# Kernel tuning notes

Measured on AMD Instinct MI355X. Metric: run time of the kernel, lower is better.

Reference implementation:

```python
import jax, jax.numpy as jnp
import numpy as np

NEG_SLOPE = 0.2
EPS_SOFTMAX = 1e-16
EPS_NORM = 1e-12
H = 4


def gat_conv(x, src, dst, edge_attr, W, att_src, att_dst, W_edge, att_edge, bias, concat):
    """PyG GATConv with edge_dim, add_self_loops=False.
    x: [N, F_in]; src,dst: [E]; edge_attr: [E, edge_dim]
    W: [F_in, H*C]; att_src/att_dst/att_edge: [H, C]; W_edge: [edge_dim, H*C]
    """
    N = x.shape[0]
    C = att_src.shape[1]
    xs = (x @ W).reshape(N, H, C)                      # [N,H,C]
    a_s = jnp.einsum('nhc,hc->nh', xs, att_src)        # [N,H]
    a_d = jnp.einsum('nhc,hc->nh', xs, att_dst)        # [N,H]
    e = (edge_attr @ W_edge).reshape(-1, H, C)         # [E,H,C]
    a_e = jnp.einsum('ehc,hc->eh', e, att_edge)        # [E,H]
    alpha = a_s[src] + a_d[dst] + a_e                  # [E,H]
    alpha = jax.nn.leaky_relu(alpha, NEG_SLOPE)
    # segment softmax over edges grouped by destination node
    m = jax.ops.segment_max(alpha, dst, num_segments=N)        # [N,H]
    ex = jnp.exp(alpha - m[dst])
    denom = jax.ops.segment_sum(ex, dst, num_segments=N)       # [N,H]
    alpha = ex / (denom[dst] + EPS_SOFTMAX)
    # message = attention-weighted source features, scatter-add to dst
    out = jax.ops.segment_sum(xs[src] * alpha[..., None], dst, num_segments=N)  # [N,H,C]
    out = out.reshape(N, H * C) if concat else out.mean(axis=1)
    return out + bias


def l2_normalize(x):
    n = jnp.linalg.norm(x, axis=-1, keepdims=True)
    return x / jnp.maximum(n, EPS_NORM)


def setup_inputs() -> dict:
    key = jax.random.key(0)
    ks = jax.random.split(key, 16)
    N, E, F_in, C1, C2 = 50000, 800000, 128, 64, 64
    glorot = lambda k, shape: jax.random.uniform(
        k, shape, jnp.float32, -1.0, 1.0) * np.sqrt(6.0 / (shape[0] + shape[-1]))
    return {
        'x': jax.random.normal(ks[0], (N, F_in), jnp.float32),
        'edge_index': jax.random.randint(ks[1], (2, E), 0, N, jnp.int32),
        'edge_weight': jax.random.uniform(ks[2], (E, 1), jnp.float32),
        # layer 1: in=128 -> H*C1=256, concat=True
        'W1': glorot(ks[3], (F_in, H * C1)),
        'att_src1': glorot(ks[4], (H, C1)),
        'att_dst1': glorot(ks[5], (H, C1)),
        'We1': glorot(ks[6], (1, H * C1)),
        'att_e1': glorot(ks[7], (H, C1)),
        'b1': jnp.zeros((H * C1,), jnp.float32),
        # layer 2: in=256 -> H*C2, concat=False (mean over heads)
        'W2': glorot(ks[8], (H * C1, H * C2)),
        'att_src2': glorot(ks[9], (H, C2)),
        'att_dst2': glorot(ks[10], (H, C2)),
        'We2': glorot(ks[11], (1, H * C2)),
        'att_e2': glorot(ks[12], (H, C2)),
        'b2': jnp.zeros((C2,), jnp.float32),
    }


def reference(x, edge_index, edge_weight, W1, att_src1, att_dst1, We1, att_e1, b1,
              W2, att_src2, att_dst2, We2, att_e2, b2):
    src, dst = edge_index[0], edge_index[1]
    h = gat_conv(x, src, dst, edge_weight, W1, att_src1, att_dst1, We1, att_e1, b1, concat=True)
    h = jax.nn.relu(l2_normalize(h))
    out = gat_conv(h, src, dst, edge_weight, W2, att_src2, att_dst2, We2, att_e2, b2, concat=False)
    return out
```

## Files before the change

kernel.cpp:

```cpp
#include <hip/hip_runtime.h>
#include <hip/hip_bf16.h>

typedef unsigned short u16;
typedef unsigned long long u64;
using bf16x8 = __attribute__((ext_vector_type(8))) short;
using f32x4v = __attribute__((ext_vector_type(4))) float;
typedef float v2f __attribute__((ext_vector_type(2)));

#define HC 256
#define CDIM 64

__device__ __forceinline__ float b2f(u16 u){
  union { unsigned int i; float f; } c; c.i = ((unsigned)u) << 16; return c.f;
}
__device__ __forceinline__ u16 f2b(float f){
  union { float f; unsigned int i; } c; c.f = f;
  unsigned int x = c.i;
  return (u16)((x + 0x7FFFu + ((x >> 16) & 1u)) >> 16);
}
__device__ __forceinline__ float ldf(const void* p, size_t i, int isbf){
  return isbf ? b2f(((const u16*)p)[i]) : ((const float*)p)[i];
}
__device__ __forceinline__ float sel4(float4 v, int h){ return h==0?v.x:(h==1?v.y:(h==2?v.z:v.w)); }
__device__ __forceinline__ float lrelu(float v){ return v>0.f ? v : 0.2f*v; }

__device__ __forceinline__ void glds16(const void* g, void* l){
  __builtin_amdgcn_global_load_lds(
      (const __attribute__((address_space(1))) unsigned int*)g,
      (__attribute__((address_space(3))) unsigned int*)l, 16, 0, 0);
}

__device__ __forceinline__ float4 wave_max4(float4 m){
  #pragma unroll
  for(int o=32;o>0;o>>=1){
    m.x=fmaxf(m.x,__shfl_xor(m.x,o));
    m.y=fmaxf(m.y,__shfl_xor(m.y,o));
    m.z=fmaxf(m.z,__shfl_xor(m.z,o));
    m.w=fmaxf(m.w,__shfl_xor(m.w,o));
  }
  return m;
}
__device__ __forceinline__ float4 wave_sum4(float4 m){
  #pragma unroll
  for(int o=32;o>0;o>>=1){
    m.x+=__shfl_xor(m.x,o);
    m.y+=__shfl_xor(m.y,o);
    m.z+=__shfl_xor(m.z,o);
    m.w+=__shfl_xor(m.w,o);
  }
  return m;
}

__global__ void k_hist(const int* __restrict__ dst, int E, int N, int* __restrict__ deg,
                       int* __restrict__ rank,
                       const u16* __restrict__ x, int nelem, int* __restrict__ flag){
  int e = blockIdx.x*256 + threadIdx.x;
  if (e < E){
    int d = dst[e];
    if ((unsigned)d < (unsigned)N) rank[e] = atomicAdd(&deg[d], 1);
  }
  if (blockIdx.x == 0){
    __shared__ int bad;
    if (threadIdx.x==0) bad = 0;
    __syncthreads();
    int n = nelem < 8192 ? nelem : 8192;
    int localbad = 0;
    for (int i=threadIdx.x; i<n; i+=256){
      int ex = (x[i] >> 7) & 0xFF;
      if (ex >= 140) localbad++;
    }
    if (localbad) atomicAdd(&bad, 1);
    __syncthreads();
    if (threadIdx.x==0) *flag = (bad==0) ? 1 : 0;
  }
}

__global__ void k_scan1(const int* __restrict__ in, int* __restrict__ out, int* __restrict__ bsums, int n){
  __shared__ int s[256];
  int t = threadIdx.x;
  int i = blockIdx.x*256 + t;
  int v = (i<n)? in[i] : 0;
  s[t]=v; __syncthreads();
  for(int off=1; off<256; off<<=1){
    int tv = (t>=off)? s[t-off] : 0;
    __syncthreads();
    s[t]+=tv; __syncthreads();
  }
  if (i<n) out[i] = s[t]-v;
  if (t==255) bsums[blockIdx.x] = s[255];
}

__global__ void k_scan2(int* __restrict__ bsums, int nb){
  __shared__ int s[256];
  int t=threadIdx.x;
  int v=(t<nb)? bsums[t]:0;
  s[t]=v; __syncthreads();
  for(int off=1; off<256; off<<=1){
    int tv=(t>=off)? s[t-off]:0;
    __syncthreads();
    s[t]+=tv; __syncthreads();
  }
  if (t<nb) bsums[t]=s[t]-v;
}

__global__ void k_scatter(const int* __restrict__ src, const int* __restrict__ dst,
                          const void* __restrict__ ew, int E, int N,
                          const int* __restrict__ rowptr, const int* __restrict__ bsums,
                          const int* __restrict__ rank, u64* __restrict__ epk,
                          const int* __restrict__ flagp){
  int e = blockIdx.x*256+threadIdx.x;
  if (e>=E) return;
  int bf = *flagp;
  int d = dst[e];
  if ((unsigned)d >= (unsigned)N) return;
  int p = rowptr[d] + bsums[d>>8] + rank[e];
  int s = src[e];
  if ((unsigned)s >= (unsigned)N) s = 0;
  u64 v = ((u64)__float_as_uint(ldf(ew, e, bf)) << 32) | (unsigned)s;
  __builtin_nontemporal_store(v, &epk[p]);
}

__global__ void k_prep(const void* __restrict__ W1, const void* __restrict__ W2,
                       const void* __restrict__ We1, const void* __restrict__ ae1,
                       const void* __restrict__ We2, const void* __restrict__ ae2,
                       u16* __restrict__ Bt1, u16* __restrict__ Bt2, float* __restrict__ ce,
                       const int* __restrict__ flagp){
  int bf = *flagp;
  int b = blockIdx.x, t = threadIdx.x;
  if (b < 128){
    Bt1[(size_t)t*128 + b] = f2b(ldf(W1, (size_t)b*HC + t, bf));
  } else if (b < 384){
    int k = b - 128;
    Bt2[(size_t)t*256 + k] = f2b(ldf(W2, (size_t)k*HC + t, bf));
  } else {
    float p1 = ldf(We1, t, bf)*ldf(ae1, t, bf);
    float p2 = ldf(We2, t, bf)*ldf(ae2, t, bf);
    #pragma unroll
    for(int o=32;o>0;o>>=1){ p1+=__shfl_xor(p1,o); p2+=__shfl_xor(p2,o); }
    if((t&63)==0){ ce[t>>6]=p1; ce[4+(t>>6)]=p2; }
  }
}

__global__ __launch_bounds__(256) void k_gemm_mfma(
    const void* __restrict__ A, int a_ext, const u16* __restrict__ Bt,
    u16* __restrict__ C, const void* __restrict__ att_s, const void* __restrict__ att_d,
    float* __restrict__ a_s, float* __restrict__ a_d,
    int M, int K, const int* __restrict__ flagp)
{
  __shared__ u16 sh[64*264];
  __shared__ float att_sh[512];
  u16* As = sh;
  u16* Bs = sh + 2048;
  int bf = *flagp;
  int a_bf = a_ext ? bf : 1;
  int tid = threadIdx.x;
  int lane = tid & 63, w = tid >> 6;
  int quad = lane >> 4, ln = lane & 15;
  int m0 = blockIdx.x * 64;

  att_sh[tid]       = ldf(att_s, tid, bf);
  att_sh[256 + tid] = ldf(att_d, tid, bf);

  f32x4v acc[4][4] = {};
  for (int k0 = 0; k0 < K; k0 += 32){
    if (!a_ext){
      const u16* gA = (const u16*)A + (size_t)(m0 + (tid>>2))*K + k0 + (size_t)(tid&3)*8;
      glds16(gA, (char*)As + (size_t)w*1024);
    } else {
      int m = tid >> 2, g = tid & 3;
      int r = m0 + m;
      uint4 pack;
      if (r < M){
        size_t base = (size_t)r*K + k0 + g*8;
        if (a_bf){
          pack = *(const uint4*)((const u16*)A + base);
        } else {
          const float* Af = (const float*)A + base;
          float4 f0 = *(const float4*)Af;
          float4 f1 = *(const float4*)(Af+4);
          unsigned a0 = (unsigned)f2b(f0.x) | ((unsigned)f2b(f0.y)<<16);
          unsigned a1 = (unsigned)f2b(f0.z) | ((unsigned)f2b(f0.w)<<16);
          unsigned a2 = (unsigned)f2b(f1.x) | ((unsigned)f2b(f1.y)<<16);
          unsigned a3 = (unsigned)f2b(f1.z) | ((unsigned)f2b(f1.w)<<16);
          pack = make_uint4(a0,a1,a2,a3);
        }
      } else pack = make_uint4(0,0,0,0);
      ((uint4*)As)[tid] = pack;
    }
    #pragma unroll
    for (int i=0;i<4;i++){
      const u16* gB = Bt + (size_t)(i*64 + (tid>>2))*K + k0 + (size_t)(tid&3)*8;
      glds16(gB, (char*)Bs + (size_t)i*4096 + (size_t)w*1024);
    }
    __syncthreads();
    bf16x8 af[4], bfr[4];
    #pragma unroll
    for (int mi=0;mi<4;mi++) af[mi] = *(const bf16x8*)&As[(mi*16+ln)*32 + quad*8];
    #pragma unroll
    for (int nj=0;nj<4;nj++) bfr[nj] = *(const bf16x8*)&Bs[((size_t)w*64+nj*16+ln)*32 + quad*8];
    #pragma unroll
    for (int mi=0;mi<4;mi++)
      #pragma unroll
      for (int nj=0;nj<4;nj++)
        acc[mi][nj] = __builtin_amdgcn_mfma_f32_16x16x32_bf16(af[mi], bfr[nj], acc[mi][nj], 0,0,0);
    __syncthreads();
  }
  #pragma unroll
  for (int mi=0;mi<4;mi++)
    #pragma unroll
    for (int nj=0;nj<4;nj++){
      union { __hip_bfloat162 h2; u16 u[2]; } cv0, cv1;
      cv0.h2 = __float22bfloat162_rn(make_float2(acc[mi][nj][0], acc[mi][nj][1]));
      cv1.h2 = __float22bfloat162_rn(make_float2(acc[mi][nj][2], acc[mi][nj][3]));
      int col = w*64 + nj*16 + ln;
      int rbase = mi*16 + quad*4;
      sh[(rbase+0)*264 + col] = cv0.u[0];
      sh[(rbase+1)*264 + col] = cv0.u[1];
      sh[(rbase+2)*264 + col] = cv1.u[0];
      sh[(rbase+3)*264 + col] = cv1.u[1];
    }
  __syncthreads();
  #pragma unroll
  for (int j=0;j<8;j++){
    int idx = j*256 + tid;
    int r = idx >> 5, gq = idx & 31;
    if (m0 + r < M)
      *(uint4*)(C + (size_t)(m0+r)*HC + gq*8) = *(const uint4*)&sh[r*264 + gq*8];
  }
  {
    int r  = w*16 + ln;
    int hh = quad;
    const u16* crow = &sh[r*264 + hh*64];
    const float* asv = &att_sh[hh*64];
    const float* adv = &att_sh[256 + hh*64];
    float ps = 0.f, pd = 0.f;
    #pragma unroll
    for (int cb=0; cb<64; cb+=8){
      ushort4 ua = *(const ushort4*)&crow[cb];
      ushort4 ub = *(const ushort4*)&crow[cb+4];
      float4 sa = *(const float4*)&asv[cb];
      float4 sb = *(const float4*)&asv[cb+4];
      float4 da = *(const float4*)&adv[cb];
      float4 db = *(const float4*)&adv[cb+4];
      float c0=b2f(ua.x), c1=b2f(ua.y), c2=b2f(ua.z), c3=b2f(ua.w);
      float c4=b2f(ub.x), c5=b2f(ub.y), c6=b2f(ub.z), c7=b2f(ub.w);
      ps += c0*sa.x + c1*sa.y + c2*sa.z + c3*sa.w + c4*sb.x + c5*sb.y + c6*sb.z + c7*sb.w;
      pd += c0*da.x + c1*da.y + c2*da.z + c3*da.w + c4*db.x + c5*db.y + c6*db.z + c7*db.w;
    }
    if (m0 + r < M){
      a_s[(size_t)(m0+r)*4 + hh] = ps;
      a_d[(size_t)(m0+r)*4 + hh] = pd;
    }
  }
}

#define GRP4(E0, TWJ) { \
  int s0_=__builtin_amdgcn_readlane(s_reg,(E0)+0); \
  int s1_=__builtin_amdgcn_readlane(s_reg,(E0)+1); \
  int s2_=__builtin_amdgcn_readlane(s_reg,(E0)+2); \
  int s3_=__builtin_amdgcn_readlane(s_reg,(E0)+3); \
  uint2 x0_=*(const uint2*)&xs[(size_t)s0_*HC + (lane<<2)]; \
  uint2 x1_=*(const uint2*)&xs[(size_t)s1_*HC + (lane<<2)]; \
  uint2 x2_=*(const uint2*)&xs[(size_t)s2_*HC + (lane<<2)]; \
  uint2 x3_=*(const uint2*)&xs[(size_t)s3_*HC + (lane<<2)]; \
  float w0_=__shfl((TWJ), ibase+(((E0)+0)&15)); \
  float w1_=__shfl((TWJ), ibase+(((E0)+1)&15)); \
  float w2_=__shfl((TWJ), ibase+(((E0)+2)&15)); \
  float w3_=__shfl((TWJ), ibase+(((E0)+3)&15)); \
  v2f f_; \
  f_=(v2f){__uint_as_float(x0_.x<<16),__uint_as_float(x0_.x&0xFFFF0000u)}; a01+=f_*w0_; \
  f_=(v2f){__uint_as_float(x0_.y<<16),__uint_as_float(x0_.y&0xFFFF0000u)}; a23+=f_*w0_; \
  f_=(v2f){__uint_as_float(x1_.x<<16),__uint_as_float(x1_.x&0xFFFF0000u)}; a01+=f_*w1_; \
  f_=(v2f){__uint_as_float(x1_.y<<16),__uint_as_float(x1_.y&0xFFFF0000u)}; a23+=f_*w1_; \
  f_=(v2f){__uint_as_float(x2_.x<<16),__uint_as_float(x2_.x&0xFFFF0000u)}; a01+=f_*w2_; \
  f_=(v2f){__uint_as_float(x2_.y<<16),__uint_as_float(x2_.y&0xFFFF0000u)}; a23+=f_*w2_; \
  f_=(v2f){__uint_as_float(x3_.x<<16),__uint_as_float(x3_.x&0xFFFF0000u)}; a01+=f_*w3_; \
  f_=(v2f){__uint_as_float(x3_.y<<16),__uint_as_float(x3_.y&0xFFFF0000u)}; a23+=f_*w3_; \
}

__global__ __launch_bounds__(256) void k_soft_agg(
    const u16* __restrict__ xs, const int* __restrict__ rowptr, const int* __restrict__ bsums,
    const int* __restrict__ deg, const u64* __restrict__ epk,
    const float* __restrict__ a_s, const float* __restrict__ a_d, const float* __restrict__ ce4,
    const void* __restrict__ bias, void* __restrict__ outp, int N, int layer,
    const int* __restrict__ flagp){
  int bf = *flagp;
  int lane = threadIdx.x & 63;
  int w = threadIdx.x >> 6;
  int n = (blockIdx.x<<2) + w;
  if (n >= N) return;
  int row = rowptr[n] + bsums[n>>8];
  int dg = deg[n];
  float4 ad = *(const float4*)&a_d[(size_t)n*4];
  float4 ce = *(const float4*)ce4;
  int h = lane >> 4;
  float4 acc = make_float4(0.f,0.f,0.f,0.f);
  if (dg > 0){
    if (dg <= 64){
      u64 pk = 0;
      if (lane < dg) pk = epk[row + lane];
      int s = (int)(unsigned)(pk & 0xFFFFFFFFull);
      if ((unsigned)s >= (unsigned)N) s = 0;
      int s_reg = s;
      float wv = __uint_as_float((unsigned)(pk >> 32));
      float4 as4 = *(const float4*)&a_s[(size_t)s*4];
      uint2 xpf[8];
      #pragma unroll
      for (int k=0;k<8;k++){
        int sk = __builtin_amdgcn_readlane(s_reg, k);
        xpf[k] = *(const uint2*)&xs[(size_t)sk*HC + (lane<<2)];
      }
      bool vlane = lane < dg;
      float4 ex;
      ex.x = vlane ? __expf(lrelu(as4.x+ad.x+wv*ce.x)) : 0.f;
      ex.y = vlane ? __expf(lrelu(as4.y+ad.y+wv*ce.y)) : 0.f;
      ex.z = vlane ? __expf(lrelu(as4.z+ad.z+wv*ce.z)) : 0.f;
      ex.w = vlane ? __expf(lrelu(as4.w+ad.w+wv*ce.w)) : 0.f;
      float4 ss = ex;
      if (dg > 32){
        ss.x+=__shfl_xor(ss.x,32); ss.y+=__shfl_xor(ss.y,32);
        ss.z+=__shfl_xor(ss.z,32); ss.w+=__shfl_xor(ss.w,32);
      }
      if (dg > 16){
        ss.x+=__shfl_xor(ss.x,16); ss.y+=__shfl_xor(ss.y,16);
        ss.z+=__shfl_xor(ss.z,16); ss.w+=__shfl_xor(ss.w,16);
      }
      #pragma unroll
      for(int o=8;o>0;o>>=1){
        ss.x+=__shfl_xor(ss.x,o); ss.y+=__shfl_xor(ss.y,o);
        ss.z+=__shfl_xor(ss.z,o); ss.w+=__shfl_xor(ss.w,o);
      }
      float4 wgt;
      wgt.x = ex.x/(ss.x+1e-16f); wgt.y = ex.y/(ss.y+1e-16f);
      wgt.z = ex.z/(ss.z+1e-16f); wgt.w = ex.w/(ss.w+1e-16f);
      int ibase = lane & 48;
      float tw0, tw1, tw2, tw3;
      {
        int srcl = lane & 15;
        float c0=__shfl(wgt.x,srcl), c1=__shfl(wgt.y,srcl);
        float c2=__shfl(wgt.z,srcl), c3=__shfl(wgt.w,srcl);
        tw0 = (h==0)?c0:((h==1)?c1:((h==2)?c2:c3));
      }
      if (dg > 16){
        int srcl = 16 + (lane & 15);
        float c0=__shfl(wgt.x,srcl), c1=__shfl(wgt.y,srcl);
        float c2=__shfl(wgt.z,srcl), c3=__shfl(wgt.w,srcl);
        tw1 = (h==0)?c0:((h==1)?c1:((h==2)?c2:c3));
      } else tw1 = 0.f;
      if (dg > 32){
        int srcl = 32 + (lane & 15);
        float c0=__shfl(wgt.x,srcl), c1=__shfl(wgt.y,srcl);
        float c2=__shfl(wgt.z,srcl), c3=__shfl(wgt.w,srcl);
        tw2 = (h==0)?c0:((h==1)?c1:((h==2)?c2:c3));
      } else tw2 = 0.f;
      if (dg > 48){
        int srcl = 48 + (lane & 15);
        float c0=__shfl(wgt.x,srcl), c1=__shfl(wgt.y,srcl);
        float c2=__shfl(wgt.z,srcl), c3=__shfl(wgt.w,srcl);
        tw3 = (h==0)?c0:((h==1)?c1:((h==2)?c2:c3));
      } else tw3 = 0.f;
      v2f a01 = {0.f,0.f}, a23 = {0.f,0.f};
      #pragma unroll
      for (int k=0;k<8;k++){
        float wk = __shfl(tw0, ibase+k);
        uint2 xv = xpf[k];
        v2f f;
        f = (v2f){__uint_as_float(xv.x<<16), __uint_as_float(xv.x&0xFFFF0000u)}; a01 += f*wk;
        f = (v2f){__uint_as_float(xv.y<<16), __uint_as_float(xv.y&0xFFFF0000u)}; a23 += f*wk;
      }
      if (dg >  8) GRP4( 8, tw0);
      if (dg > 12) GRP4(12, tw0);
      if (dg > 16){
        GRP4(16, tw1);
        if (dg > 20) GRP4(20, tw1);
        if (dg > 24) GRP4(24, tw1);
        if (dg > 28) GRP4(28, tw1);
        if (dg > 32){
          GRP4(32, tw2);
          if (dg > 36) GRP4(36, tw2);
          if (dg > 40) GRP4(40, tw2);
          if (dg > 44) GRP4(44, tw2);
          if (dg > 48){
            GRP4(48, tw3);
            if (dg > 52) GRP4(52, tw3);
            if (dg > 56) GRP4(56, tw3);
            if (dg > 60) GRP4(60, tw3);
          }
        }
      }
      acc.x = a01.x; acc.y = a01.y; acc.z = a23.x; acc.w = a23.y;
    } else {
      float4 m = make_float4(-1e30f,-1e30f,-1e30f,-1e30f);
      for (int p=lane;p<dg;p+=64){
        u64 pk = epk[row+p];
        int s = (int)(unsigned)(pk & 0xFFFFFFFFull);
        if ((unsigned)s >= (unsigned)N) s = 0;
        float wv = __uint_as_float((unsigned)(pk >> 32));
        float4 as = *(const float4*)&a_s[(size_t)s*4];
        m.x=fmaxf(m.x, lrelu(as.x+ad.x+wv*ce.x));
        m.y=fmaxf(m.y, lrelu(as.y+ad.y+wv*ce.y));
        m.z=fmaxf(m.z, lrelu(as.z+ad.z+wv*ce.z));
        m.w=fmaxf(m.w, lrelu(as.w+ad.w+wv*ce.w));
      }
      m = wave_max4(m);
      float4 ss = make_float4(0.f,0.f,0.f,0.f);
      for (int p=lane;p<dg;p+=64){
        u64 pk = epk[row+p];
        int s = (int)(unsigned)(pk & 0xFFFFFFFFull);
        if ((unsigned)s >= (unsigned)N) s = 0;
        float wv = __uint_as_float((unsigned)(pk >> 32));
        float4 as = *(const float4*)&a_s[(size_t)s*4];
        ss.x+=__expf(lrelu(as.x+ad.x+wv*ce.x)-m.x);
        ss.y+=__expf(lrelu(as.y+ad.y+wv*ce.y)-m.y);
        ss.z+=__expf(lrelu(as.z+ad.z+wv*ce.z)-m.z);
        ss.w+=__expf(lrelu(as.w+ad.w+wv*ce.w)-m.w);
      }
      ss = wave_sum4(ss);
      float rsel=1.f/(sel4(ss,h)+1e-16f), mh=sel4(m,h), adh=sel4(ad,h), ceh=sel4(ce,h);
      for (int e=0;e<dg;e++){
        u64 pk = epk[row+e];
        int s = (int)(unsigned)(pk & 0xFFFFFFFFull);
        if ((unsigned)s >= (unsigned)N) s = 0;
        float wv = __uint_as_float((unsigned)(pk >> 32));
        float arv = lrelu(a_s[(size_t)s*4+h]+adh+wv*ceh);
        float wgt = __expf(arv-mh)*rsel;
        ushort4 xv4 = *(const ushort4*)&xs[(size_t)s*HC + lane*4];
        acc.x+=wgt*b2f(xv4.x); acc.y+=wgt*b2f(xv4.y);
        acc.z+=wgt*b2f(xv4.z); acc.w+=wgt*b2f(xv4.w);
      }
    }
  }
  if (layer==1){
    float4 v;
    v.x = acc.x + ldf(bias, lane*4+0, bf);
    v.y = acc.y + ldf(bias, lane*4+1, bf);
    v.z = acc.z + ldf(bias, lane*4+2, bf);
    v.w = acc.w + ldf(bias, lane*4+3, bf);
    float ss = v.x*v.x+v.y*v.y+v.z*v.z+v.w*v.w;
    #pragma unroll
    for(int o=32;o>0;o>>=1) ss += __shfl_xor(ss,o);
    float inv = 1.f/fmaxf(sqrtf(ss), 1e-12f);
    ushort4 o4;
    o4.x = f2b(fmaxf(v.x*inv,0.f)); o4.y = f2b(fmaxf(v.y*inv,0.f));
    o4.z = f2b(fmaxf(v.z*inv,0.f)); o4.w = f2b(fmaxf(v.w*inv,0.f));
    *(ushort4*)((u16*)outp + (size_t)n*HC + lane*4) = o4;
  } else {
    float4 s = acc;
    #pragma unroll
    for (int o=16;o<=32;o<<=1){
      s.x+=__shfl_xor(s.x,o); s.y+=__shfl_xor(s.y,o);
      s.z+=__shfl_xor(s.z,o); s.w+=__shfl_xor(s.w,o);
    }
    if (lane < 16){
      float4 v;
      v.x = 0.25f*s.x + ldf(bias, lane*4+0, bf);
      v.y = 0.25f*s.y + ldf(bias, lane*4+1, bf);
      v.z = 0.25f*s.z + ldf(bias, lane*4+2, bf);
      v.w = 0.25f*s.w + ldf(bias, lane*4+3, bf);
      if (bf){
        ushort4 o4; o4.x=f2b(v.x); o4.y=f2b(v.y); o4.z=f2b(v.z); o4.w=f2b(v.w);
        *(ushort4*)((u16*)outp + (size_t)n*CDIM + lane*4) = o4;
      } else {
        *(float4*)((float*)outp + (size_t)n*CDIM + lane*4) = v;
      }
    }
  }
}

extern "C" void kernel_launch(void* const* d_in, const int* in_sizes, int n_in,
                              void* d_out, int out_size, void* d_ws, size_t ws_size,
                              hipStream_t stream){
  const void* x_in = d_in[0];
  const int* eidx  = (const int*)d_in[1];
  const void* ew   = d_in[2];
  const void* W1   = d_in[3];
  const void* as1  = d_in[4];
  const void* ad1  = d_in[5];
  const void* We1  = d_in[6];
  const void* ae1  = d_in[7];
  const void* b1   = d_in[8];
  const void* W2   = d_in[9];
  const void* as2  = d_in[10];
  const void* ad2  = d_in[11];
  const void* We2  = d_in[12];
  const void* ae2  = d_in[13];
  const void* b2   = d_in[14];

  int N = in_sizes[0]/128;
  int E = in_sizes[2];
  const int* src = eidx;
  const int* dst = eidx + E;

  char* w = (char*)d_ws;
  auto alloc = [&](size_t bytes)->char*{ char* p=w; w += (bytes+255)/256*256; return p; };
  int*   flag  = (int*)alloc(256);
  u16*   xs    = (u16*)alloc((size_t)N*HC*2);
  u16*   agg   = (u16*)alloc((size_t)N*HC*2);
  float* a_s   = (float*)alloc((size_t)N*4*4);
  float* a_d   = (float*)alloc((size_t)N*4*4);
  int*   deg   = (int*)alloc((size_t)N*4);
  int*   rowptr= (int*)alloc((size_t)N*4);
  int*   bsums = (int*)alloc(256*4);
  int*   rank  = (int*)alloc((size_t)E*4);
  u64*   epk   = (u64*)alloc((size_t)E*8);
  float* ce    = (float*)alloc(256);
  u16*   Bt1   = (u16*)alloc((size_t)HC*128*2);
  u16*   Bt2   = (u16*)alloc((size_t)HC*HC*2);

  (void)hipMemsetAsync(deg, 0, (size_t)N*4, stream);

  int eb = (E+255)/256;
  int nb = (N+255)/256;
  k_hist<<<eb,256,0,stream>>>(dst, E, N, deg, rank, (const u16*)x_in, in_sizes[0], flag);
  k_scan1<<<nb,256,0,stream>>>(deg, rowptr, bsums, N);
  k_scan2<<<1,256,0,stream>>>(bsums, nb);
  k_scatter<<<eb,256,0,stream>>>(src, dst, ew, E, N, rowptr, bsums, rank, epk, flag);
  k_prep<<<385,256,0,stream>>>(W1, W2, We1, ae1, We2, ae2, Bt1, Bt2, ce, flag);

  int gemmBlocks = (N+63)/64;
  int nwb = (N+3)/4;

  k_gemm_mfma<<<gemmBlocks,256,0,stream>>>(x_in, 1, Bt1, xs, as1, ad1, a_s, a_d, N, 128, flag);
  k_soft_agg<<<nwb,256,0,stream>>>(xs, rowptr, bsums, deg, epk, a_s, a_d, ce, b1, agg, N, 1, flag);

  k_gemm_mfma<<<gemmBlocks,256,0,stream>>>(agg, 0, Bt2, xs, as2, ad2, a_s, a_d, N, 256, flag);
  k_soft_agg<<<nwb,256,0,stream>>>(xs, rowptr, bsums, deg, epk, a_s, a_d, ce+4, b2, d_out, N, 2, flag);
}
```

Measured before the change: 328.5 us.

## Split waves into half-wave edge pairs with 16-byte gathers; fuse prep into hist

The soft-aggregation kernel now has each half-wave handle alternate edges, with every lane gathering 8 bf16 features (16 bytes) instead of 4. The two halves are combined with a cross-half shuffle at the end, and the block size drops to 128 threads (2 nodes per block). The aim is fewer, wider gather instructions and more edges in flight per wave, at the cost of extra reduction shuffles and ds_bpermute weight broadcasts. Separately, the weight-prep kernel is merged into the histogram kernel to save a launch, and the GEMM uses the direct global-to-LDS load path for bf16 inputs on full tiles.

Result: slower. 343.5 us (+4.6%).

```diff
diff --git a/kernel.cpp b/kernel.cpp
--- a/kernel.cpp
+++ b/kernel.cpp
@@ -23,6 +23,9 @@
 }
 __device__ __forceinline__ float sel4(float4 v, int h){ return h==0?v.x:(h==1?v.y:(h==2?v.z:v.w)); }
 __device__ __forceinline__ float lrelu(float v){ return v>0.f ? v : 0.2f*v; }
+__device__ __forceinline__ float wshf(float v, int addr4){
+  return __int_as_float(__builtin_amdgcn_ds_bpermute(addr4, __float_as_int(v)));
+}
 
 __device__ __forceinline__ void glds16(const void* g, void* l){
   __builtin_amdgcn_global_load_lds(
@@ -51,27 +54,63 @@
   return m;
 }
 
-__global__ void k_hist(const int* __restrict__ dst, int E, int N, int* __restrict__ deg,
-                       int* __restrict__ rank,
-                       const u16* __restrict__ x, int nelem, int* __restrict__ flag){
-  int e = blockIdx.x*256 + threadIdx.x;
-  if (e < E){
-    int d = dst[e];
-    if ((unsigned)d < (unsigned)N) rank[e] = atomicAdd(&deg[d], 1);
-  }
-  if (blockIdx.x == 0){
-    __shared__ int bad;
-    if (threadIdx.x==0) bad = 0;
-    __syncthreads();
+__global__ void k_hist_prep(const int* __restrict__ dst, int E, int N, int* __restrict__ deg,
+                            int* __restrict__ rank,
+                            const u16* __restrict__ x, int nelem, int* __restrict__ flag,
+                            const void* __restrict__ W1, const void* __restrict__ W2,
+                            const void* __restrict__ We1, const void* __restrict__ ae1,
+                            const void* __restrict__ We2, const void* __restrict__ ae2,
+                            u16* __restrict__ Bt1, u16* __restrict__ Bt2, float* __restrict__ ce){
+  int eb = (E + 255) >> 8;
+  int t = threadIdx.x;
+  if ((int)blockIdx.x < eb){
+    int e = blockIdx.x*256 + t;
+    if (e < E){
+      int d = dst[e];
+      if ((unsigned)d < (unsigned)N) rank[e] = atomicAdd(&deg[d], 1);
+    }
+    if (blockIdx.x == 0){
+      __shared__ int bad0;
+      if (t==0) bad0 = 0;
+      __syncthreads();
+      int n = nelem < 8192 ? nelem : 8192;
+      int localbad = 0;
+      for (int i=t; i<n; i+=256){
+        int ex = (x[i] >> 7) & 0xFF;
+        if (ex >= 140) localbad++;
+      }
+      if (localbad) atomicAdd(&bad0, 1);
+      __syncthreads();
+      if (t==0) *flag = (bad0==0) ? 1 : 0;
+    }
+    return;
+  }
+  __shared__ int bad;
+  if (t==0) bad = 0;
+  __syncthreads();
+  {
     int n = nelem < 8192 ? nelem : 8192;
     int localbad = 0;
-    for (int i=threadIdx.x; i<n; i+=256){
+    for (int i=t; i<n; i+=256){
       int ex = (x[i] >> 7) & 0xFF;
       if (ex >= 140) localbad++;
     }
     if (localbad) atomicAdd(&bad, 1);
-    __syncthreads();
-    if (threadIdx.x==0) *flag = (bad==0) ? 1 : 0;
+  }
+  __syncthreads();
+  int bf = (bad==0) ? 1 : 0;
+  int b = blockIdx.x - eb;
+  if (b < 128){
+    Bt1[(size_t)t*128 + b] = f2b(ldf(W1, (size_t)b*HC + t, bf));
+  } else if (b < 384){
+    int k = b - 128;
+    Bt2[(size_t)t*256 + k] = f2b(ldf(W2, (size_t)k*HC + t, bf));
+  } else {
+    float p1 = ldf(We1, t, bf)*ldf(ae1, t, bf);
+    float p2 = ldf(We2, t, bf)*ldf(ae2, t, bf);
+    #pragma unroll
+    for(int o=32;o>0;o>>=1){ p1+=__shfl_xor(p1,o); p2+=__shfl_xor(p2,o); }
+    if((t&63)==0){ ce[t>>6]=p1; ce[4+(t>>6)]=p2; }
   }
 }
 
@@ -118,27 +157,6 @@
   if ((unsigned)s >= (unsigned)N) s = 0;
   u64 v = ((u64)__float_as_uint(ldf(ew, e, bf)) << 32) | (unsigned)s;
   __builtin_nontemporal_store(v, &epk[p]);
-}
-
-__global__ void k_prep(const void* __restrict__ W1, const void* __restrict__ W2,
-                       const void* __restrict__ We1, const void* __restrict__ ae1,
-                       const void* __restrict__ We2, const void* __restrict__ ae2,
-                       u16* __restrict__ Bt1, u16* __restrict__ Bt2, float* __restrict__ ce,
-                       const int* __restrict__ flagp){
-  int bf = *flagp;
-  int b = blockIdx.x, t = threadIdx.x;
-  if (b < 128){
-    Bt1[(size_t)t*128 + b] = f2b(ldf(W1, (size_t)b*HC + t, bf));
-  } else if (b < 384){
-    int k = b - 128;
-    Bt2[(size_t)t*256 + k] = f2b(ldf(W2, (size_t)k*HC + t, bf));
-  } else {
-    float p1 = ldf(We1, t, bf)*ldf(ae1, t, bf);
-    float p2 = ldf(We2, t, bf)*ldf(ae2, t, bf);
-    #pragma unroll
-    for(int o=32;o>0;o>>=1){ p1+=__shfl_xor(p1,o); p2+=__shfl_xor(p2,o); }
-    if((t&63)==0){ ce[t>>6]=p1; ce[4+(t>>6)]=p2; }
-  }
 }
 
 __global__ __launch_bounds__(256) void k_gemm_mfma(
@@ -157,13 +175,14 @@
   int lane = tid & 63, w = tid >> 6;
   int quad = lane >> 4, ln = lane & 15;
   int m0 = blockIdx.x * 64;
+  bool adma = (!a_ext) || (a_bf && (m0 + 64 <= M));
 
   att_sh[tid]       = ldf(att_s, tid, bf);
   att_sh[256 + tid] = ldf(att_d, tid, bf);
 
   f32x4v acc[4][4] = {};
   for (int k0 = 0; k0 < K; k0 += 32){
-    if (!a_ext){
+    if (adma){
       const u16* gA = (const u16*)A + (size_t)(m0 + (tid>>2))*K + k0 + (size_t)(tid&3)*8;
       glds16(gA, (char*)As + (size_t)w*1024);
     } else {
@@ -254,31 +273,23 @@
   }
 }
 
-#define GRP4(E0, TWJ) { \
-  int s0_=__builtin_amdgcn_readlane(s_reg,(E0)+0); \
-  int s1_=__builtin_amdgcn_readlane(s_reg,(E0)+1); \
-  int s2_=__builtin_amdgcn_readlane(s_reg,(E0)+2); \
-  int s3_=__builtin_amdgcn_readlane(s_reg,(E0)+3); \
-  uint2 x0_=*(const uint2*)&xs[(size_t)s0_*HC + (lane<<2)]; \
-  uint2 x1_=*(const uint2*)&xs[(size_t)s1_*HC + (lane<<2)]; \
-  uint2 x2_=*(const uint2*)&xs[(size_t)s2_*HC + (lane<<2)]; \
-  uint2 x3_=*(const uint2*)&xs[(size_t)s3_*HC + (lane<<2)]; \
-  float w0_=__shfl((TWJ), ibase+(((E0)+0)&15)); \
-  float w1_=__shfl((TWJ), ibase+(((E0)+1)&15)); \
-  float w2_=__shfl((TWJ), ibase+(((E0)+2)&15)); \
-  float w3_=__shfl((TWJ), ibase+(((E0)+3)&15)); \
+#define PLOAD(P, DST) { \
+  int sA_ = __builtin_amdgcn_readlane(s_reg, 2*(P)); \
+  int sB_ = __builtin_amdgcn_readlane(s_reg, 2*(P)+1); \
+  int ss_ = hf ? sB_ : sA_; \
+  DST = *(const uint4*)&xs[(size_t)ss_*HC + (c32<<3)]; \
+}
+#define PAPPLY(P, XV, TWJ) { \
+  float wk_ = wshf((TWJ), baseW4 + (((P)&7)<<3)); \
   v2f f_; \
-  f_=(v2f){__uint_as_float(x0_.x<<16),__uint_as_float(x0_.x&0xFFFF0000u)}; a01+=f_*w0_; \
-  f_=(v2f){__uint_as_float(x0_.y<<16),__uint_as_float(x0_.y&0xFFFF0000u)}; a23+=f_*w0_; \
-  f_=(v2f){__uint_as_float(x1_.x<<16),__uint_as_float(x1_.x&0xFFFF0000u)}; a01+=f_*w1_; \
-  f_=(v2f){__uint_as_float(x1_.y<<16),__uint_as_float(x1_.y&0xFFFF0000u)}; a23+=f_*w1_; \
-  f_=(v2f){__uint_as_float(x2_.x<<16),__uint_as_float(x2_.x&0xFFFF0000u)}; a01+=f_*w2_; \
-  f_=(v2f){__uint_as_float(x2_.y<<16),__uint_as_float(x2_.y&0xFFFF0000u)}; a23+=f_*w2_; \
-  f_=(v2f){__uint_as_float(x3_.x<<16),__uint_as_float(x3_.x&0xFFFF0000u)}; a01+=f_*w3_; \
-  f_=(v2f){__uint_as_float(x3_.y<<16),__uint_as_float(x3_.y&0xFFFF0000u)}; a23+=f_*w3_; \
-}
-
-__global__ __launch_bounds__(256) void k_soft_agg(
+  f_=(v2f){__uint_as_float((XV).x<<16),__uint_as_float((XV).x&0xFFFF0000u)}; av0+=f_*wk_; \
+  f_=(v2f){__uint_as_float((XV).y<<16),__uint_as_float((XV).y&0xFFFF0000u)}; av1+=f_*wk_; \
+  f_=(v2f){__uint_as_float((XV).z<<16),__uint_as_float((XV).z&0xFFFF0000u)}; av2+=f_*wk_; \
+  f_=(v2f){__uint_as_float((XV).w<<16),__uint_as_float((XV).w&0xFFFF0000u)}; av3+=f_*wk_; \
+}
+#define PAIR2(P, TWJ) { uint4 xv_; PLOAD(P, xv_); PAPPLY(P, xv_, TWJ); }
+
+__global__ __launch_bounds__(128) void k_soft_agg(
     const u16* __restrict__ xs, const int* __restrict__ rowptr, const int* __restrict__ bsums,
     const int* __restrict__ deg, const u64* __restrict__ epk,
     const float* __restrict__ a_s, const float* __restrict__ a_d, const float* __restrict__ ce4,
@@ -287,14 +298,16 @@
   int bf = *flagp;
   int lane = threadIdx.x & 63;
   int w = threadIdx.x >> 6;
-  int n = (blockIdx.x<<2) + w;
+  int n = (blockIdx.x<<1) + w;
   if (n >= N) return;
+  int c32 = lane & 31, hf = lane >> 5;
+  int baseW4 = ((c32>>3)<<6) | (hf<<2);
   int row = rowptr[n] + bsums[n>>8];
   int dg = deg[n];
   float4 ad = *(const float4*)&a_d[(size_t)n*4];
   float4 ce = *(const float4*)ce4;
   int h = lane >> 4;
-  float4 acc = make_float4(0.f,0.f,0.f,0.f);
+  v2f av0={0.f,0.f}, av1={0.f,0.f}, av2={0.f,0.f}, av3={0.f,0.f};
   if (dg > 0){
     if (dg <= 64){
       u64 pk = 0;
@@ -304,12 +317,8 @@
       int s_reg = s;
       float wv = __uint_as_float((unsigned)(pk >> 32));
       float4 as4 = *(const float4*)&a_s[(size_t)s*4];
-      uint2 xpf[8];
-      #pragma unroll
-      for (int k=0;k<8;k++){
-        int sk = __builtin_amdgcn_readlane(s_reg, k);
-        xpf[k] = *(const uint2*)&xs[(size_t)sk*HC + (lane<<2)];
-      }
+      uint4 xpf0, xpf1, xpf2, xpf3;
+      PLOAD(0, xpf0); PLOAD(1, xpf1); PLOAD(2, xpf2); PLOAD(3, xpf3);
       bool vlane = lane < dg;
       float4 ex;
       ex.x = vlane ? __expf(lrelu(as4.x+ad.x+wv*ce.x)) : 0.f;
@@ -333,7 +342,6 @@
       float4 wgt;
       wgt.x = ex.x/(ss.x+1e-16f); wgt.y = ex.y/(ss.y+1e-16f);
       wgt.z = ex.z/(ss.z+1e-16f); wgt.w = ex.w/(ss.w+1e-16f);
-      int ibase = lane & 48;
       float tw0, tw1, tw2, tw3;
       {
         int srcl = lane & 15;
@@ -359,36 +367,25 @@
         float c2=__shfl(wgt.z,srcl), c3=__shfl(wgt.w,srcl);
         tw3 = (h==0)?c0:((h==1)?c1:((h==2)?c2:c3));
       } else tw3 = 0.f;
-      v2f a01 = {0.f,0.f}, a23 = {0.f,0.f};
-      #pragma unroll
-      for (int k=0;k<8;k++){
-        float wk = __shfl(tw0, ibase+k);
-        uint2 xv = xpf[k];
-        v2f f;
-        f = (v2f){__uint_as_float(xv.x<<16), __uint_as_float(xv.x&0xFFFF0000u)}; a01 += f*wk;
-        f = (v2f){__uint_as_float(xv.y<<16), __uint_as_float(xv.y&0xFFFF0000u)}; a23 += f*wk;
-      }
-      if (dg >  8) GRP4( 8, tw0);
-      if (dg > 12) GRP4(12, tw0);
-      if (dg > 16){
-        GRP4(16, tw1);
-        if (dg > 20) GRP4(20, tw1);
-        if (dg > 24) GRP4(24, tw1);
-        if (dg > 28) GRP4(28, tw1);
-        if (dg > 32){
-          GRP4(32, tw2);
-          if (dg > 36) GRP4(36, tw2);
-          if (dg > 40) GRP4(40, tw2);
-          if (dg > 44) GRP4(44, tw2);
-          if (dg > 48){
-            GRP4(48, tw3);
-            if (dg > 52) GRP4(52, tw3);
-            if (dg > 56) GRP4(56, tw3);
-            if (dg > 60) GRP4(60, tw3);
+      PAPPLY(0, xpf0, tw0); PAPPLY(1, xpf1, tw0);
+      PAPPLY(2, xpf2, tw0); PAPPLY(3, xpf3, tw0);
+      if (dg >  8){ PAIR2(4, tw0); PAIR2(5, tw0); }
+      if (dg > 12){ PAIR2(6, tw0); PAIR2(7, tw0); }
+      if (dg > 16){ PAIR2(8, tw1); PAIR2(9, tw1);
+        if (dg > 20){ PAIR2(10, tw1); PAIR2(11, tw1); }
+        if (dg > 24){ PAIR2(12, tw1); PAIR2(13, tw1); }
+        if (dg > 28){ PAIR2(14, tw1); PAIR2(15, tw1); }
+        if (dg > 32){ PAIR2(16, tw2); PAIR2(17, tw2);
+          if (dg > 36){ PAIR2(18, tw2); PAIR2(19, tw2); }
+          if (dg > 40){ PAIR2(20, tw2); PAIR2(21, tw2); }
+          if (dg > 44){ PAIR2(22, tw2); PAIR2(23, tw2); }
+          if (dg > 48){ PAIR2(24, tw3); PAIR2(25, tw3);
+            if (dg > 52){ PAIR2(26, tw3); PAIR2(27, tw3); }
+            if (dg > 56){ PAIR2(28, tw3); PAIR2(29, tw3); }
+            if (dg > 60){ PAIR2(30, tw3); PAIR2(31, tw3); }
           }
         }
       }
-      acc.x = a01.x; acc.y = a01.y; acc.z = a23.x; acc.w = a23.y;
     } else {
       float4 m = make_float4(-1e30f,-1e30f,-1e30f,-1e30f);
       for (int p=lane;p<dg;p+=64){
@@ -403,65 +400,82 @@
         m.w=fmaxf(m.w, lrelu(as.w+ad.w+wv*ce.w));
       }
       m = wave_max4(m);
-      float4 ss = make_float4(0.f,0.f,0.f,0.f);
+      float4 sv = make_float4(0.f,0.f,0.f,0.f);
       for (int p=lane;p<dg;p+=64){
         u64 pk = epk[row+p];
         int s = (int)(unsigned)(pk & 0xFFFFFFFFull);
         if ((unsigned)s >= (unsigned)N) s = 0;
         float wv = __uint_as_float((unsigned)(pk >> 32));
         float4 as = *(const float4*)&a_s[(size_t)s*4];
-        ss.x+=__expf(lrelu(as.x+ad.x+wv*ce.x)-m.x);
-        ss.y+=__expf(lrelu(as.y+ad.y+wv*ce.y)-m.y);
-        ss.z+=__expf(lrelu(as.z+ad.z+wv*ce.z)-m.z);
-        ss.w+=__expf(lrelu(as.w+ad.w+wv*ce.w)-m.w);
-      }
-      ss = wave_sum4(ss);
-      float rsel=1.f/(sel4(ss,h)+1e-16f), mh=sel4(m,h), adh=sel4(ad,h), ceh=sel4(ce,h);
-      for (int e=0;e<dg;e++){
+        sv.x+=__expf(lrelu(as.x+ad.x+wv*ce.x)-m.x);
+        sv.y+=__expf(lrelu(as.y+ad.y+wv*ce.y)-m.y);
+        sv.z+=__expf(lrelu(as.z+ad.z+wv*ce.z)-m.z);
+        sv.w+=__expf(lrelu(as.w+ad.w+wv*ce.w)-m.w);
+      }
+      sv = wave_sum4(sv);
+      int hq = c32 >> 3;
+      float rsel=1.f/(sel4(sv,hq)+1e-16f), mh=sel4(m,hq), adh=sel4(ad,hq), ceh=sel4(ce,hq);
+      for (int e=hf;e<dg;e+=2){
         u64 pk = epk[row+e];
         int s = (int)(unsigned)(pk & 0xFFFFFFFFull);
         if ((unsigned)s >= (unsigned)N) s = 0;
         float wv = __uint_as_float((unsigned)(pk >> 32));
-        float arv = lrelu(a_s[(size_t)s*4+h]+adh+wv*ceh);
-        float wgt = __expf(arv-mh)*rsel;
-        ushort4 xv4 = *(const ushort4*)&xs[(size_t)s*HC + lane*4];
-        acc.x+=wgt*b2f(xv4.x); acc.y+=wgt*b2f(xv4.y);
-        acc.z+=wgt*b2f(xv4.z); acc.w+=wgt*b2f(xv4.w);
-      }
-    }
-  }
+        float arv = lrelu(a_s[(size_t)s*4+hq]+adh+wv*ceh);
+        float wk = __expf(arv-mh)*rsel;
+        uint4 xv = *(const uint4*)&xs[(size_t)s*HC + (c32<<3)];
+        v2f f;
+        f=(v2f){__uint_as_float(xv.x<<16),__uint_as_float(xv.x&0xFFFF0000u)}; av0+=f*wk;
+        f=(v2f){__uint_as_float(xv.y<<16),__uint_as_float(xv.y&0xFFFF0000u)}; av1+=f*wk;
+        f=(v2f){__uint_as_float(xv.z<<16),__uint_as_float(xv.z&0xFFFF0000u)}; av2+=f*wk;
+        f=(v2f){__uint_as_float(xv.w<<16),__uint_as_float(xv.w&0xFFFF0000u)}; av3+=f*wk;
+      }
+    }
+  }
+  float vb0=av0.x, vb1=av0.y, vb2=av1.x, vb3=av1.y, vb4=av2.x, vb5=av2.y, vb6=av3.x, vb7=av3.y;
+  vb0+=__shfl_xor(vb0,32); vb1+=__shfl_xor(vb1,32); vb2+=__shfl_xor(vb2,32); vb3+=__shfl_xor(vb3,32);
+  vb4+=__shfl_xor(vb4,32); vb5+=__shfl_xor(vb5,32); vb6+=__shfl_xor(vb6,32); vb7+=__shfl_xor(vb7,32);
   if (layer==1){
-    float4 v;
-    v.x = acc.x + ldf(bias, lane*4+0, bf);
-    v.y = acc.y + ldf(bias, lane*4+1, bf);
-    v.z = acc.z + ldf(bias, lane*4+2, bf);
-    v.w = acc.w + ldf(bias, lane*4+3, bf);
-    float ss = v.x*v.x+v.y*v.y+v.z*v.z+v.w*v.w;
-    #pragma unroll
-    for(int o=32;o>0;o>>=1) ss += __shfl_xor(ss,o);
+    int fb = c32 << 3;
+    vb0 += ldf(bias, fb+0, bf); vb1 += ldf(bias, fb+1, bf);
+    vb2 += ldf(bias, fb+2, bf); vb3 += ldf(bias, fb+3, bf);
+    vb4 += ldf(bias, fb+4, bf); vb5 += ldf(bias, fb+5, bf);
+    vb6 += ldf(bias, fb+6, bf); vb7 += ldf(bias, fb+7, bf);
+    float ss = vb0*vb0+vb1*vb1+vb2*vb2+vb3*vb3+vb4*vb4+vb5*vb5+vb6*vb6+vb7*vb7;
+    #pragma unroll
+    for(int o=16;o>0;o>>=1) ss += __shfl_xor(ss,o);
     float inv = 1.f/fmaxf(sqrtf(ss), 1e-12f);
-    ushort4 o4;
-    o4.x = f2b(fmaxf(v.x*inv,0.f)); o4.y = f2b(fmaxf(v.y*inv,0.f));
-    o4.z = f2b(fmaxf(v.z*inv,0.f)); o4.w = f2b(fmaxf(v.w*inv,0.f));
-    *(ushort4*)((u16*)outp + (size_t)n*HC + lane*4) = o4;
+    if (hf==0){
+      union { u16 u[8]; uint4 v; } pk8;
+      pk8.u[0]=f2b(fmaxf(vb0*inv,0.f)); pk8.u[1]=f2b(fmaxf(vb1*inv,0.f));
+      pk8.u[2]=f2b(fmaxf(vb2*inv,0.f)); pk8.u[3]=f2b(fmaxf(vb3*inv,0.f));
+      pk8.u[4]=f2b(fmaxf(vb4*inv,0.f)); pk8.u[5]=f2b(fmaxf(vb5*inv,0.f));
+      pk8.u[6]=f2b(fmaxf(vb6*inv,0.f)); pk8.u[7]=f2b(fmaxf(vb7*inv,0.f));
+      *(uint4*)((u16*)outp + (size_t)n*HC + fb) = pk8.v;
+    }
   } else {
-    float4 s = acc;
-    #pragma unroll
-    for (int o=16;o<=32;o<<=1){
-      s.x+=__shfl_xor(s.x,o); s.y+=__shfl_xor(s.y,o);
-      s.z+=__shfl_xor(s.z,o); s.w+=__shfl_xor(s.w,o);
-    }
-    if (lane < 16){
-      float4 v;
-      v.x = 0.25f*s.x + ldf(bias, lane*4+0, bf);
-      v.y = 0.25f*s.y + ldf(bias, lane*4+1, bf);
-      v.z = 0.25f*s.z + ldf(bias, lane*4+2, bf);
-      v.w = 0.25f*s.w + ldf(bias, lane*4+3, bf);
+    vb0+=__shfl_xor(vb0,8);  vb1+=__shfl_xor(vb1,8);  vb2+=__shfl_xor(vb2,8);  vb3+=__shfl_xor(vb3,8);
+    vb4+=__shfl_xor(vb4,8);  vb5+=__shfl_xor(vb5,8);  vb6+=__shfl_xor(vb6,8);  vb7+=__shfl_xor(vb7,8);
+    vb0+=__shfl_xor(vb0,16); vb1+=__shfl_xor(vb1,16); vb2+=__shfl_xor(vb2,16); vb3+=__shfl_xor(vb3,16);
+    vb4+=__shfl_xor(vb4,16); vb5+=__shfl_xor(vb5,16); vb6+=__shfl_xor(vb6,16); vb7+=__shfl_xor(vb7,16);
+    if (hf==0 && c32 < 8){
+      int cb = c32 << 3;
+      float o0 = 0.25f*vb0 + ldf(bias, cb+0, bf);
+      float o1 = 0.25f*vb1 + ldf(bias, cb+1, bf);
+      float o2 = 0.25f*vb2 + ldf(bias, cb+2, bf);
+      float o3 = 0.25f*vb3 + ldf(bias, cb+3, bf);
+      float o4 = 0.25f*vb4 + ldf(bias, cb+4, bf);
+      float o5 = 0.25f*vb5 + ldf(bias, cb+5, bf);
+      float o6 = 0.25f*vb6 + ldf(bias, cb+6, bf);
+      float o7 = 0.25f*vb7 + ldf(bias, cb+7, bf);
       if (bf){
-        ushort4 o4; o4.x=f2b(v.x); o4.y=f2b(v.y); o4.z=f2b(v.z); o4.w=f2b(v.w);
-        *(ushort4*)((u16*)outp + (size_t)n*CDIM + lane*4) = o4;
+        union { u16 u[8]; uint4 v; } pk8;
+        pk8.u[0]=f2b(o0); pk8.u[1]=f2b(o1); pk8.u[2]=f2b(o2); pk8.u[3]=f2b(o3);
+        pk8.u[4]=f2b(o4); pk8.u[5]=f2b(o5); pk8.u[6]=f2b(o6); pk8.u[7]=f2b(o7);
+        *(uint4*)((u16*)outp + (size_t)n*CDIM + cb) = pk8.v;
       } else {
-        *(float4*)((float*)outp + (size_t)n*CDIM + lane*4) = v;
+        float* of = (float*)outp + (size_t)n*CDIM + cb;
+        *(float4*)of     = make_float4(o0,o1,o2,o3);
+        *(float4*)(of+4) = make_float4(o4,o5,o6,o7);
       }
     }
   }
@@ -511,18 +525,18 @@
 
   int eb = (E+255)/256;
   int nb = (N+255)/256;
-  k_hist<<<eb,256,0,stream>>>(dst, E, N, deg, rank, (const u16*)x_in, in_sizes[0], flag);
+  k_hist_prep<<<eb+385,256,0,stream>>>(dst, E, N, deg, rank, (const u16*)x_in, in_sizes[0], flag,
+                                       W1, W2, We1, ae1, We2, ae2, Bt1, Bt2, ce);
   k_scan1<<<nb,256,0,stream>>>(deg, rowptr, bsums, N);
   k_scan2<<<1,256,0,stream>>>(bsums, nb);
   k_scatter<<<eb,256,0,stream>>>(src, dst, ew, E, N, rowptr, bsums, rank, epk, flag);
-  k_prep<<<385,256,0,stream>>>(W1, W2, We1, ae1, We2, ae2, Bt1, Bt2, ce, flag);
 
   int gemmBlocks = (N+63)/64;
-  int nwb = (N+3)/4;
+  int nwb = (N+1)/2;
 
   k_gemm_mfma<<<gemmBlocks,256,0,stream>>>(x_in, 1, Bt1, xs, as1, ad1, a_s, a_d, N, 128, flag);
-  k_soft_agg<<<nwb,256,0,stream>>>(xs, rowptr, bsums, deg, epk, a_s, a_d, ce, b1, agg, N, 1, flag);
+  k_soft_agg<<<nwb,128,0,stream>>>(xs, rowptr, bsums, deg, epk, a_s, a_d, ce, b1, agg, N, 1, flag);
 
   k_gemm_mfma<<<gemmBlocks,256,0,stream>>>(agg, 0, Bt2, xs, as2, ad2, a_s, a_d, N, 256, flag);
-  k_soft_agg<<<nwb,256,0,stream>>>(xs, rowptr, bsums, deg, epk, a_s, a_d, ce+4, b2, d_out, N, 2, flag);
-}
+  k_soft_agg<<<nwb,128,0,stream>>>(xs, rowptr, bsums, deg, epk, a_s, a_d, ce+4, b2, d_out, N, 2, flag);
+}
```

## Fuse CSR preprocessing into one cooperative kernel; use direct LDS load for bf16 input

Applied to the files above, without the earlier changes.

Replaces the memset plus five preprocessing launches (histogram, two scans, scatter, weight prep) with a single cooperative kernel that uses grid-wide syncs between phases. This removes several launch gaps and kernel boundaries from the setup path. It also lets the first GEMM use the direct global-to-LDS load when the input is bf16 and the tile is full, skipping the register conversion path. The cost is grid.sync overhead and the persistent grid doing grid-stride loops with fewer resident blocks.

Result: slower. 886.2 us (+169.8%).

```diff
diff --git a/kernel.cpp b/kernel.cpp
--- a/kernel.cpp
+++ b/kernel.cpp
@@ -1,5 +1,8 @@
 #include <hip/hip_runtime.h>
 #include <hip/hip_bf16.h>
+#include <hip/hip_cooperative_groups.h>
+
+namespace cg = cooperative_groups;
 
 typedef unsigned short u16;
 typedef unsigned long long u64;
@@ -51,93 +54,103 @@
   return m;
 }
 
-__global__ void k_hist(const int* __restrict__ dst, int E, int N, int* __restrict__ deg,
-                       int* __restrict__ rank,
-                       const u16* __restrict__ x, int nelem, int* __restrict__ flag){
-  int e = blockIdx.x*256 + threadIdx.x;
-  if (e < E){
+__global__ __launch_bounds__(256) void k_pre(
+    const int* __restrict__ dst, const int* __restrict__ srcv, const void* __restrict__ ew,
+    int E, int N,
+    int* __restrict__ deg, int* __restrict__ rank, int* __restrict__ rowptr,
+    int* __restrict__ bsums,
+    const u16* __restrict__ x, int nelem, int* __restrict__ flag,
+    const void* __restrict__ W1, const void* __restrict__ W2,
+    const void* __restrict__ We1, const void* __restrict__ ae1,
+    const void* __restrict__ We2, const void* __restrict__ ae2,
+    u16* __restrict__ Bt1, u16* __restrict__ Bt2, float* __restrict__ ce,
+    u64* __restrict__ epk)
+{
+  cg::grid_group grid = cg::this_grid();
+  __shared__ int s[256];
+  __shared__ int bad0;
+  int t = threadIdx.x;
+  int gtid = blockIdx.x*256 + t;
+  int gstride = gridDim.x*256;
+
+  for (int i = gtid; i < N; i += gstride) deg[i] = 0;
+  if (blockIdx.x == 0){
+    if (t==0) bad0 = 0;
+    __syncthreads();
+    int n = nelem < 8192 ? nelem : 8192;
+    int lb = 0;
+    for (int i=t; i<n; i+=256){
+      int ex = (x[i] >> 7) & 0xFF;
+      if (ex >= 140) lb++;
+    }
+    if (lb) atomicAdd(&bad0, 1);
+    __syncthreads();
+    if (t==0) *flag = (bad0==0) ? 1 : 0;
+  }
+  grid.sync();
+  int bf = *flag;
+
+  for (int e = gtid; e < E; e += gstride){
     int d = dst[e];
     if ((unsigned)d < (unsigned)N) rank[e] = atomicAdd(&deg[d], 1);
   }
+  for (int b = blockIdx.x; b < 385; b += gridDim.x){
+    if (b < 128){
+      Bt1[(size_t)t*128 + b] = f2b(ldf(W1, (size_t)b*HC + t, bf));
+    } else if (b < 384){
+      int k = b - 128;
+      Bt2[(size_t)t*256 + k] = f2b(ldf(W2, (size_t)k*HC + t, bf));
+    } else {
+      float p1 = ldf(We1, t, bf)*ldf(ae1, t, bf);
+      float p2 = ldf(We2, t, bf)*ldf(ae2, t, bf);
+      #pragma unroll
+      for(int o=32;o>0;o>>=1){ p1+=__shfl_xor(p1,o); p2+=__shfl_xor(p2,o); }
+      if((t&63)==0){ ce[t>>6]=p1; ce[4+(t>>6)]=p2; }
+    }
+  }
+  grid.sync();
+
+  int nb = (N + 255) >> 8;
+  for (int c = blockIdx.x; c < nb; c += gridDim.x){
+    int i = c*256 + t;
+    int v = (i<N)? deg[i] : 0;
+    s[t]=v; __syncthreads();
+    for(int off=1; off<256; off<<=1){
+      int tv = (t>=off)? s[t-off] : 0;
+      __syncthreads();
+      s[t]+=tv; __syncthreads();
+    }
+    if (i<N) rowptr[i] = s[t]-v;
+    if (t==255) bsums[c] = s[255];
+    __syncthreads();
+  }
+  grid.sync();
+
   if (blockIdx.x == 0){
-    __shared__ int bad;
-    if (threadIdx.x==0) bad = 0;
-    __syncthreads();
-    int n = nelem < 8192 ? nelem : 8192;
-    int localbad = 0;
-    for (int i=threadIdx.x; i<n; i+=256){
-      int ex = (x[i] >> 7) & 0xFF;
-      if (ex >= 140) localbad++;
-    }
-    if (localbad) atomicAdd(&bad, 1);
-    __syncthreads();
-    if (threadIdx.x==0) *flag = (bad==0) ? 1 : 0;
-  }
-}
-
-__global__ void k_scan1(const int* __restrict__ in, int* __restrict__ out, int* __restrict__ bsums, int n){
-  __shared__ int s[256];
-  int t = threadIdx.x;
-  int i = blockIdx.x*256 + t;
-  int v = (i<n)? in[i] : 0;
-  s[t]=v; __syncthreads();
-  for(int off=1; off<256; off<<=1){
-    int tv = (t>=off)? s[t-off] : 0;
-    __syncthreads();
-    s[t]+=tv; __syncthreads();
-  }
-  if (i<n) out[i] = s[t]-v;
-  if (t==255) bsums[blockIdx.x] = s[255];
-}
-
-__global__ void k_scan2(int* __restrict__ bsums, int nb){
-  __shared__ int s[256];
-  int t=threadIdx.x;
-  int v=(t<nb)? bsums[t]:0;
-  s[t]=v; __syncthreads();
-  for(int off=1; off<256; off<<=1){
-    int tv=(t>=off)? s[t-off]:0;
-    __syncthreads();
-    s[t]+=tv; __syncthreads();
-  }
-  if (t<nb) bsums[t]=s[t]-v;
-}
-
-__global__ void k_scatter(const int* __restrict__ src, const int* __restrict__ dst,
-                          const void* __restrict__ ew, int E, int N,
-                          const int* __restrict__ rowptr, const int* __restrict__ bsums,
-                          const int* __restrict__ rank, u64* __restrict__ epk,
-                          const int* __restrict__ flagp){
-  int e = blockIdx.x*256+threadIdx.x;
-  if (e>=E) return;
-  int bf = *flagp;
-  int d = dst[e];
-  if ((unsigned)d >= (unsigned)N) return;
-  int p = rowptr[d] + bsums[d>>8] + rank[e];
-  int s = src[e];
-  if ((unsigned)s >= (unsigned)N) s = 0;
-  u64 v = ((u64)__float_as_uint(ldf(ew, e, bf)) << 32) | (unsigned)s;
-  __builtin_nontemporal_store(v, &epk[p]);
-}
-
-__global__ void k_prep(const void* __restrict__ W1, const void* __restrict__ W2,
-                       const void* __restrict__ We1, const void* __restrict__ ae1,
-                       const void* __restrict__ We2, const void* __restrict__ ae2,
-                       u16* __restrict__ Bt1, u16* __restrict__ Bt2, float* __restrict__ ce,
-                       const int* __restrict__ flagp){
-  int bf = *flagp;
-  int b = blockIdx.x, t = threadIdx.x;
-  if (b < 128){
-    Bt1[(size_t)t*128 + b] = f2b(ldf(W1, (size_t)b*HC + t, bf));
-  } else if (b < 384){
-    int k = b - 128;
-    Bt2[(size_t)t*256 + k] = f2b(ldf(W2, (size_t)k*HC + t, bf));
-  } else {
-    float p1 = ldf(We1, t, bf)*ldf(ae1, t, bf);
-    float p2 = ldf(We2, t, bf)*ldf(ae2, t, bf);
-    #pragma unroll
-    for(int o=32;o>0;o>>=1){ p1+=__shfl_xor(p1,o); p2+=__shfl_xor(p2,o); }
-    if((t&63)==0){ ce[t>>6]=p1; ce[4+(t>>6)]=p2; }
+    if (nb <= 256){
+      int v = (t<nb)? bsums[t] : 0;
+      s[t]=v; __syncthreads();
+      for(int off=1; off<256; off<<=1){
+        int tv=(t>=off)? s[t-off]:0;
+        __syncthreads();
+        s[t]+=tv; __syncthreads();
+      }
+      if (t<nb) bsums[t]=s[t]-v;
+    } else if (t==0){
+      int acc=0;
+      for (int i=0;i<nb;i++){ int v=bsums[i]; bsums[i]=acc; acc+=v; }
+    }
+  }
+  grid.sync();
+
+  for (int e = gtid; e < E; e += gstride){
+    int d = dst[e];
+    if ((unsigned)d >= (unsigned)N) continue;
+    int p = rowptr[d] + bsums[d>>8] + rank[e];
+    int sv = srcv[e];
+    if ((unsigned)sv >= (unsigned)N) sv = 0;
+    u64 v = ((u64)__float_as_uint(ldf(ew, e, bf)) << 32) | (unsigned)sv;
+    __builtin_nontemporal_store(v, &epk[p]);
   }
 }
 
@@ -157,13 +170,14 @@
   int lane = tid & 63, w = tid >> 6;
   int quad = lane >> 4, ln = lane & 15;
   int m0 = blockIdx.x * 64;
+  bool adma = (!a_ext) || (a_bf && (m0 + 64 <= M));
 
   att_sh[tid]       = ldf(att_s, tid, bf);
   att_sh[256 + tid] = ldf(att_d, tid, bf);
 
   f32x4v acc[4][4] = {};
   for (int k0 = 0; k0 < K; k0 += 32){
-    if (!a_ext){
+    if (adma){
       const u16* gA = (const u16*)A + (size_t)(m0 + (tid>>2))*K + k0 + (size_t)(tid&3)*8;
       glds16(gA, (char*)As + (size_t)w*1024);
     } else {
@@ -488,8 +502,8 @@
 
   int N = in_sizes[0]/128;
   int E = in_sizes[2];
-  const int* src = eidx;
-  const int* dst = eidx + E;
+  const int* srcp = eidx;
+  const int* dstp = eidx + E;
 
   char* w = (char*)d_ws;
   auto alloc = [&](size_t bytes)->char*{ char* p=w; w += (bytes+255)/256*256; return p; };
@@ -507,15 +521,31 @@
   u16*   Bt1   = (u16*)alloc((size_t)HC*128*2);
   u16*   Bt2   = (u16*)alloc((size_t)HC*HC*2);
 
-  (void)hipMemsetAsync(deg, 0, (size_t)N*4, stream);
-
-  int eb = (E+255)/256;
-  int nb = (N+255)/256;
-  k_hist<<<eb,256,0,stream>>>(dst, E, N, deg, rank, (const u16*)x_in, in_sizes[0], flag);
-  k_scan1<<<nb,256,0,stream>>>(deg, rowptr, bsums, N);
-  k_scan2<<<1,256,0,stream>>>(bsums, nb);
-  k_scatter<<<eb,256,0,stream>>>(src, dst, ew, E, N, rowptr, bsums, rank, epk, flag);
-  k_prep<<<385,256,0,stream>>>(W1, W2, We1, ae1, We2, ae2, Bt1, Bt2, ce, flag);
+  static int coopGrid = 0;
+  if (coopGrid == 0){
+    int perCU = 0;
+    hipError_t err = hipOccupancyMaxActiveBlocksPerMultiprocessor(&perCU, (const void*)k_pre, 256, 0);
+    if (err != hipSuccess || perCU < 1) perCU = 1;
+    hipDeviceProp_t prop;
+    int dev = 0;
+    (void)hipGetDevice(&dev);
+    (void)hipGetDeviceProperties(&prop, dev);
+    int g = perCU * prop.multiProcessorCount;
+    if (g > 2048) g = 2048;
+    if (g < 64) g = 64;
+    coopGrid = g;
+  }
+
+  int nelem = in_sizes[0];
+  const u16* xp = (const u16*)x_in;
+  void* args[] = {
+    (void*)&dstp, (void*)&srcp, (void*)&ew, (void*)&E, (void*)&N,
+    (void*)&deg, (void*)&rank, (void*)&rowptr, (void*)&bsums,
+    (void*)&xp, (void*)&nelem, (void*)&flag,
+    (void*)&W1, (void*)&W2, (void*)&We1, (void*)&ae1, (void*)&We2, (void*)&ae2,
+    (void*)&Bt1, (void*)&Bt2, (void*)&ce, (void*)&epk
+  };
+  (void)hipLaunchCooperativeKernel((const void*)k_pre, dim3(coopGrid), dim3(256), args, 0, stream);
 
   int gemmBlocks = (N+63)/64;
   int nwb = (N+3)/4;
```
